# Performance work log

Hardware: AMD Instinct MI355X
Metric: run time of the kernel (lower is better)

Reference implementation:

```python
import jax, jax.numpy as jnp
import numpy as np

TEMPERATURE = 0.5

def setup_inputs() -> dict:
    key = jax.random.key(0)
    k1, k2, k3 = jax.random.split(key, 3)
    B, C, T = 32, 64, 4096
    M, D = 512, 64
    x = jax.random.normal(k1, (B, C, T), dtype=jnp.float32)
    u = jax.random.uniform(k2, (B, T, M), dtype=jnp.float32)
    # nn.init.uniform_(weight, -1/M, 1/M)
    weight = jax.random.uniform(k3, (M, D), dtype=jnp.float32,
                                minval=-1.0 / M, maxval=1.0 / M)
    return {"x": x, "u": u, "weight": weight}

def reference(x, u, weight):
    B, C, T = x.shape
    M, D = weight.shape
    xt = jnp.transpose(x, (0, 2, 1))            # (B, T, D)
    x_flat = xt.reshape(-1, D)                  # (B*T, D)
    distances = (jnp.sum(weight ** 2, axis=1)[None, :]
                 + jnp.sum(x_flat ** 2, axis=1, keepdims=True)
                 - 2.0 * (x_flat @ weight.T)).reshape(B, T, M)
    logits = -distances
    # RelaxedOneHotCategorical(0.5, logits).rsample()
    uu = jnp.clip(u, 1e-9, 1.0 - 1e-9)
    gumbel = -jnp.log(-jnp.log(uu))
    samples = jax.nn.softmax((logits + gumbel) / TEMPERATURE, axis=-1)  # (B,T,M)
    quantized = samples @ weight                # (B, T, D)
    # KL to uniform prior: probs * (log_probs + log M), zero where probs == 0
    log_probs = jax.nn.log_softmax(logits, axis=-1)
    probs = jnp.exp(log_probs)
    KL = jnp.where(probs == 0, 0.0, probs * (log_probs + jnp.log(jnp.float32(M))))
    KL = jnp.mean(jnp.sum(KL, axis=(1, 2)))
    avg_probs = jnp.mean(samples, axis=(0, 1))  # (M,)
    perplexity = jnp.exp(-jnp.sum(avg_probs * jnp.log(avg_probs + 1e-10)))
    return quantized, KL, perplexity
```

## Files before the change

kernel.cpp:

```cpp
#include <hip/hip_runtime.h>
#include <hip/hip_bf16.h>
#include <math.h>


#define LOG_M   6.2383246250395075f
#define EXPM36  2.3195228e-16f

typedef __attribute__((ext_vector_type(8))) __bf16 bf16x8;
typedef __attribute__((ext_vector_type(4))) float  floatx4;

__device__ __forceinline__ unsigned int f2bf_bits(float f) {
    unsigned int b = __builtin_bit_cast(unsigned int, f);
    return (b + 0x7fffu + ((b >> 16) & 1u)) >> 16;
}
__device__ __forceinline__ float bf2f(unsigned int bits16) {
    return __builtin_bit_cast(float, bits16 << 16);
}

__global__ void vq_prep(const float* __restrict__ W,
                        unsigned short* __restrict__ Wbf,
                        unsigned short* __restrict__ WTbf,
                        float* __restrict__ wn2)
{
    const int m = blockIdx.x * 256 + threadIdx.x;
    float acc = 0.f;
    #pragma unroll 8
    for (int d = 0; d < 64; ++d) {
        float v = W[m * 64 + d];
        acc = fmaf(v, v, acc);
        unsigned short h = (unsigned short)f2bf_bits(v);
        Wbf[m * 64 + d]  = h;
        WTbf[d * 512 + m] = h;
    }
    wn2[m] = acc;
}

__global__ __launch_bounds__(256, 3) void vq_main(
    const float* __restrict__ x, const float* __restrict__ u,
    const unsigned short* __restrict__ Wbf, const unsigned short* __restrict__ WTbf,
    const float* __restrict__ wn2, float* __restrict__ out,
    float* __restrict__ avg_g, float* __restrict__ kl_g)
{
    __shared__ __align__(16) unsigned short xs[64][72];
    __shared__ __align__(16) unsigned short sbuf[4][16][40];
    __shared__ float avg_lds[512];

    const int tid  = threadIdx.x;
    const int bid  = blockIdx.x;
    const int b    = bid >> 6;
    const int t0   = (bid & 63) << 6;
    const int w    = tid >> 6;
    const int lane = tid & 63;
    const int ln   = lane & 15;
    const int q    = lane >> 4;

    avg_lds[tid]       = 0.0f;
    avg_lds[tid + 256] = 0.0f;

    #pragma unroll
    for (int k2 = 0; k2 < 16; ++k2) {
        int idx = k2 * 256 + tid;
        int d = idx >> 6, t = idx & 63;
        float v = x[((size_t)(b * 64 + d)) * 4096 + (size_t)(t0 + t)];
        xs[t][d] = (unsigned short)f2bf_bits(v);
    }
    __syncthreads();

    const int tg = t0 + 16 * w + ln;

    bf16x8 xb0 = *(const bf16x8*)&xs[16 * w + ln][q * 8];
    bf16x8 xb1 = *(const bf16x8*)&xs[16 * w + ln][32 + q * 8];

    unsigned int spk[64];
    float T1 = 0.f, T2 = 0.f, Zg = 0.f;
    const float* ub = u + ((size_t)(b * 4096 + tg)) * 512 + 4 * q;

    #pragma unroll
    for (int i = 0; i < 32; ++i) {
        const unsigned short* wrow = Wbf + (size_t)(16 * i + ln) * 64 + q * 8;
        bf16x8 a0 = *(const bf16x8*)(wrow);
        bf16x8 a1 = *(const bf16x8*)(wrow + 32);
        float4 uv = *(const float4*)(ub + 16 * i);
        const float4 wv = *(const float4*)(wn2 + 16 * i + 4 * q);

        floatx4 acc = 0.0f;
        acc = __builtin_amdgcn_mfma_f32_16x16x32_bf16(a0, xb0, acc, 0, 0, 0);
        acc = __builtin_amdgcn_mfma_f32_16x16x32_bf16(a1, xb1, acc, 0, 0, 0);

        float sr[4];
        const float ua[4] = {uv.x, uv.y, uv.z, uv.w};
        const float wa[4] = {wv.x, wv.y, wv.z, wv.w};
        #pragma unroll
        for (int r = 0; r < 4; ++r) {
            float l = fmaf(2.0f, acc[r], -wa[r]);
            float e = __expf(l);
            T1 += e;
            T2 = fmaf(l, e, T2);
            float uu = fmaxf(ua[r], 1e-9f);
            float z = uu - 1.0f;
            float p = fmaf(z, -0.125f, 0.14285715f);
            p = fmaf(z, p, -0.16666667f);
            p = fmaf(z, p, 0.2f);
            p = fmaf(z, p, -0.25f);
            p = fmaf(z, p, 0.33333334f);
            p = fmaf(z, p, -0.5f);
            p = fmaf(z, p, 1.0f);
            float il = (uu > 0.75f) ? (z * p) : __logf(uu);
            float rr = e * __builtin_amdgcn_rcpf(il);
            float s = (rr * rr) * EXPM36;
            Zg += s;
            sr[r] = s;
        }
        spk[2 * i]     = f2bf_bits(sr[0]) | (f2bf_bits(sr[1]) << 16);
        spk[2 * i + 1] = f2bf_bits(sr[2]) | (f2bf_bits(sr[3]) << 16);
    }

    T1 += __shfl_xor(T1, 16); T1 += __shfl_xor(T1, 32);
    T2 += __shfl_xor(T2, 16); T2 += __shfl_xor(T2, 32);
    Zg += __shfl_xor(Zg, 16); Zg += __shfl_xor(Zg, 32);

    float klw = T2 / T1 - logf(T1) + LOG_M;
    klw += __shfl_xor(klw, 1);  klw += __shfl_xor(klw, 2);
    klw += __shfl_xor(klw, 4);  klw += __shfl_xor(klw, 8);
    klw += __shfl_xor(klw, 16); klw += __shfl_xor(klw, 32);
    if (lane == 0) atomicAdd(kl_g, 0.25f * klw);

    const float invZ = 1.0f / Zg;

    floatx4 C2[4];
    #pragma unroll
    for (int dt = 0; dt < 4; ++dt) C2[dt] = 0.0f;

    #pragma unroll
    for (int kk = 0; kk < 16; ++kk) {
        #pragma unroll
        for (int ii = 0; ii < 2; ++ii) {
            const int i = 2 * kk + ii;
            uint2 pk;
            pk.x = spk[2 * i];
            pk.y = spk[2 * i + 1];
            *(uint2*)&sbuf[w][ln][16 * ii + 4 * q] = pk;
            float v0 = bf2f(pk.x & 0xffffu) * invZ;
            float v1 = bf2f(pk.x >> 16)     * invZ;
            float v2 = bf2f(pk.y & 0xffffu) * invZ;
            float v3 = bf2f(pk.y >> 16)     * invZ;
            v0 += __shfl_xor(v0,1); v0 += __shfl_xor(v0,2); v0 += __shfl_xor(v0,4); v0 += __shfl_xor(v0,8);
            v1 += __shfl_xor(v1,1); v1 += __shfl_xor(v1,2); v1 += __shfl_xor(v1,4); v1 += __shfl_xor(v1,8);
            v2 += __shfl_xor(v2,1); v2 += __shfl_xor(v2,2); v2 += __shfl_xor(v2,4); v2 += __shfl_xor(v2,8);
            v3 += __shfl_xor(v3,1); v3 += __shfl_xor(v3,2); v3 += __shfl_xor(v3,4); v3 += __shfl_xor(v3,8);
            if (ln == 0) {
                atomicAdd(&avg_lds[16*i + 4*q + 0], v0);
                atomicAdd(&avg_lds[16*i + 4*q + 1], v1);
                atomicAdd(&avg_lds[16*i + 4*q + 2], v2);
                atomicAdd(&avg_lds[16*i + 4*q + 3], v3);
            }
        }
        __asm__ volatile("s_waitcnt lgkmcnt(0)" ::: "memory");
        bf16x8 sb = *(const bf16x8*)&sbuf[w][ln][8 * q];
        #pragma unroll
        for (int dt = 0; dt < 4; ++dt) {
            bf16x8 a = *(const bf16x8*)(WTbf + (size_t)(16 * dt + ln) * 512 + 32 * kk + 8 * q);
            C2[dt] = __builtin_amdgcn_mfma_f32_16x16x32_bf16(a, sb, C2[dt], 0, 0, 0);
        }
    }

    float* op = out + ((size_t)(b * 4096 + tg)) * 64 + 4 * q;
    #pragma unroll
    for (int dt = 0; dt < 4; ++dt) {
        floatx4 c = C2[dt];
        c[0] *= invZ; c[1] *= invZ; c[2] *= invZ; c[3] *= invZ;
        *(floatx4*)(op + 16 * dt) = c;
    }

    __syncthreads();
    atomicAdd(&avg_g[tid],       avg_lds[tid]);
    atomicAdd(&avg_g[tid + 256], avg_lds[tid + 256]);
}

__global__ void vq_fin(const float* __restrict__ avg_g, const float* __restrict__ kl_g,
                       float* __restrict__ out)
{
    const int lane = threadIdx.x;
    float acc = 0.f;
    #pragma unroll
    for (int k = 0; k < 8; ++k) {
        float a = avg_g[lane * 8 + k] * (1.0f / 131072.0f);
        acc += a * logf(a + 1e-10f);
    }
    acc += __shfl_xor(acc, 1);  acc += __shfl_xor(acc, 2);
    acc += __shfl_xor(acc, 4);  acc += __shfl_xor(acc, 8);
    acc += __shfl_xor(acc, 16); acc += __shfl_xor(acc, 32);
    if (lane == 0) {
        out[8388608] = kl_g[0] * (1.0f / 32.0f);
        out[8388609] = expf(-acc);
    }
}

extern "C" void kernel_launch(void* const* d_in, const int* in_sizes, int n_in,
                              void* d_out, int out_size, void* d_ws, size_t ws_size,
                              hipStream_t stream)
{
    const float* x = (const float*)d_in[0];
    const float* u = (const float*)d_in[1];
    const float* W = (const float*)d_in[2];
    float* out = (float*)d_out;

    char* ws = (char*)d_ws;
    unsigned short* Wbf  = (unsigned short*)(ws);
    unsigned short* WTbf = (unsigned short*)(ws + 65536);
    float* wn2   = (float*)(ws + 131072);
    float* avg_g = (float*)(ws + 133120);
    float* kl_g  = (float*)(ws + 135168);

    (void)hipMemsetAsync(ws + 133120, 0, 2048 + 64, stream);

    vq_prep<<<dim3(2),    dim3(256), 0, stream>>>(W, Wbf, WTbf, wn2);
    vq_main<<<dim3(2048), dim3(256), 0, stream>>>(x, u, Wbf, WTbf, wn2, out, avg_g, kl_g);
    vq_fin <<<dim3(1),    dim3(64),  0, stream>>>(avg_g, kl_g, out);
}
```

Measured before the change: 570.1 us.

## Split fused VQ kernel into sampling and quantize passes via global buffer

The single fused kernel is split in two. The first kernel computes the Gumbel-softmax samples and writes them as bf16 to a large workspace buffer, along with per-row inverse normalizers. The second kernel reads them back to run the quantize matmul and the codebook-average reduction. This removes the 64-register packed sample array and the 3-waves launch bound, aiming for higher occupancy. The cost is about 256MB of extra global write and read traffic. It also swaps shuffle reductions for DPP row sums, shards the global atomics across 16 slots, and replaces the memset with zeroing inside the prep kernel. The new path only runs when the workspace is large enough; otherwise the old fused path is kept.

```diff
diff --git a/kernel.cpp b/kernel.cpp
--- a/kernel.cpp
+++ b/kernel.cpp
@@ -16,11 +16,27 @@
 __device__ __forceinline__ float bf2f(unsigned int bits16) {
     return __builtin_bit_cast(float, bits16 << 16);
 }
+template <int CTRL>
+__device__ __forceinline__ float dpp_add(float v) {
+    int t = __builtin_amdgcn_update_dpp(0, __builtin_bit_cast(int, v),
+                                        CTRL, 0xF, 0xF, true);
+    return v + __builtin_bit_cast(float, t);
+}
+__device__ __forceinline__ float row16_sum(float v) {
+    v = dpp_add<0xB1>(v);
+    v = dpp_add<0x4E>(v);
+    v = dpp_add<0x124>(v);
+    v = dpp_add<0x128>(v);
+    return v;
+}
 
 __global__ void vq_prep(const float* __restrict__ W,
                         unsigned short* __restrict__ Wbf,
                         unsigned short* __restrict__ WTbf,
-                        float* __restrict__ wn2)
+                        float* __restrict__ wn2,
+                        float* __restrict__ avg_sh,
+                        float* __restrict__ kl_sh,
+                        int zero_mode)
 {
     const int m = blockIdx.x * 256 + threadIdx.x;
     float acc = 0.f;
@@ -33,6 +49,206 @@
         WTbf[d * 512 + m] = h;
     }
     wn2[m] = acc;
+    if (zero_mode) {
+        #pragma unroll
+        for (int j = 0; j < 16; ++j) avg_sh[m * 16 + j] = 0.f;
+        kl_sh[m * 2]     = 0.f;
+        kl_sh[m * 2 + 1] = 0.f;
+    }
+}
+
+__global__ __launch_bounds__(256, 4) void vq_samp(
+    const float* __restrict__ x, const float* __restrict__ u,
+    const unsigned short* __restrict__ Wbf,
+    const float* __restrict__ wn2,
+    unsigned short* __restrict__ Sblk,
+    float* __restrict__ invZg,
+    float* __restrict__ kl_sh)
+{
+    __shared__ __align__(16) unsigned short xs[64][72];
+    __shared__ __align__(16) unsigned short sbuf[4][16][40];
+
+    const int tid  = threadIdx.x;
+    const int bid  = blockIdx.x;
+    const int b    = bid >> 6;
+    const int t0   = (bid & 63) << 6;
+    const int w    = tid >> 6;
+    const int lane = tid & 63;
+    const int ln   = lane & 15;
+    const int q    = lane >> 4;
+
+    #pragma unroll
+    for (int k2 = 0; k2 < 16; ++k2) {
+        int idx = k2 * 256 + tid;
+        int d = idx >> 6, t = idx & 63;
+        float v = x[((size_t)(b * 64 + d)) * 4096 + (size_t)(t0 + t)];
+        xs[t][d] = (unsigned short)f2bf_bits(v);
+    }
+    __syncthreads();
+
+    const int tg = t0 + 16 * w + ln;
+
+    bf16x8 xb0 = *(const bf16x8*)&xs[16 * w + ln][q * 8];
+    bf16x8 xb1 = *(const bf16x8*)&xs[16 * w + ln][32 + q * 8];
+
+    float T1 = 0.f, T2 = 0.f, Zg = 0.f;
+    const float* ub = u + ((size_t)(b * 4096 + tg)) * 512 + 4 * q;
+
+    #pragma unroll 2
+    for (int kk = 0; kk < 16; ++kk) {
+        #pragma unroll
+        for (int ii = 0; ii < 2; ++ii) {
+            const int i = 2 * kk + ii;
+            const unsigned short* wrow = Wbf + (size_t)(16 * i + ln) * 64 + q * 8;
+            bf16x8 a0 = *(const bf16x8*)(wrow);
+            bf16x8 a1 = *(const bf16x8*)(wrow + 32);
+            float4 uv = *(const float4*)(ub + 16 * i);
+            const float4 wv = *(const float4*)(wn2 + 16 * i + 4 * q);
+
+            floatx4 acc = 0.0f;
+            acc = __builtin_amdgcn_mfma_f32_16x16x32_bf16(a0, xb0, acc, 0, 0, 0);
+            acc = __builtin_amdgcn_mfma_f32_16x16x32_bf16(a1, xb1, acc, 0, 0, 0);
+
+            float sr[4];
+            const float ua[4] = {uv.x, uv.y, uv.z, uv.w};
+            const float wa[4] = {wv.x, wv.y, wv.z, wv.w};
+            #pragma unroll
+            for (int r = 0; r < 4; ++r) {
+                float l = fmaf(2.0f, acc[r], -wa[r]);
+                float e = __expf(l);
+                T1 += e;
+                T2 = fmaf(l, e, T2);
+                float uu = fmaxf(ua[r], 1e-9f);
+                float z = uu - 1.0f;
+                float p = fmaf(z, -0.125f, 0.14285715f);
+                p = fmaf(z, p, -0.16666667f);
+                p = fmaf(z, p, 0.2f);
+                p = fmaf(z, p, -0.25f);
+                p = fmaf(z, p, 0.33333334f);
+                p = fmaf(z, p, -0.5f);
+                p = fmaf(z, p, 1.0f);
+                float il = (uu > 0.75f) ? (z * p) : __logf(uu);
+                float rr = e * __builtin_amdgcn_rcpf(il);
+                float s = (rr * rr) * EXPM36;
+                Zg += s;
+                sr[r] = s;
+            }
+            *(uint2*)&sbuf[w][ln][16 * ii + 4 * q] = make_uint2(
+                f2bf_bits(sr[0]) | (f2bf_bits(sr[1]) << 16),
+                f2bf_bits(sr[2]) | (f2bf_bits(sr[3]) << 16));
+        }
+        __asm__ volatile("s_waitcnt lgkmcnt(0)" ::: "memory");
+        uint4 sv = *(const uint4*)&sbuf[w][ln][8 * q];
+        *(uint4*)(Sblk + (((size_t)bid * 16 + kk) * 4 + w) * 512 + lane * 8) = sv;
+    }
+
+    T1 += __shfl_xor(T1, 16); T1 += __shfl_xor(T1, 32);
+    T2 += __shfl_xor(T2, 16); T2 += __shfl_xor(T2, 32);
+    Zg += __shfl_xor(Zg, 16); Zg += __shfl_xor(Zg, 32);
+
+    float klw = T2 / T1 - logf(T1) + LOG_M;
+    klw += __shfl_xor(klw, 1);  klw += __shfl_xor(klw, 2);
+    klw += __shfl_xor(klw, 4);  klw += __shfl_xor(klw, 8);
+    klw += __shfl_xor(klw, 16); klw += __shfl_xor(klw, 32);
+    if (lane == 0)
+        atomicAdd(&kl_sh[((bid * 4 + w) & 15) * 64], 0.25f * klw);
+
+    if (q == 0) invZg[(size_t)b * 4096 + tg] = 1.0f / Zg;
+}
+
+__global__ __launch_bounds__(256, 4) void vq_qnt(
+    const unsigned short* __restrict__ Sblk,
+    const unsigned short* __restrict__ WTbf,
+    const float* __restrict__ invZg,
+    float* __restrict__ out,
+    float* __restrict__ avg_sh)
+{
+    __shared__ float avg_wv[4][512];
+
+    const int tid  = threadIdx.x;
+    const int bid  = blockIdx.x;
+    const int b    = bid >> 6;
+    const int t0   = (bid & 63) << 6;
+    const int w    = tid >> 6;
+    const int lane = tid & 63;
+    const int ln   = lane & 15;
+    const int q    = lane >> 4;
+    const int tg   = t0 + 16 * w + ln;
+
+    const float invZ = invZg[(size_t)b * 4096 + tg];
+
+    floatx4 C2[4];
+    #pragma unroll
+    for (int dt = 0; dt < 4; ++dt) C2[dt] = 0.0f;
+
+    #pragma unroll 4
+    for (int kk = 0; kk < 16; ++kk) {
+        uint4 sv = *(const uint4*)(Sblk + (((size_t)bid * 16 + kk) * 4 + w) * 512 + lane * 8);
+        bf16x8 sb = __builtin_bit_cast(bf16x8, sv);
+
+        float p0 = bf2f(sv.x & 0xffffu) * invZ;
+        float p1 = bf2f(sv.x >> 16)     * invZ;
+        float p2 = bf2f(sv.y & 0xffffu) * invZ;
+        float p3 = bf2f(sv.y >> 16)     * invZ;
+        float p4 = bf2f(sv.z & 0xffffu) * invZ;
+        float p5 = bf2f(sv.z >> 16)     * invZ;
+        float p6 = bf2f(sv.w & 0xffffu) * invZ;
+        float p7 = bf2f(sv.w >> 16)     * invZ;
+        p0 = row16_sum(p0); p1 = row16_sum(p1); p2 = row16_sum(p2); p3 = row16_sum(p3);
+        p4 = row16_sum(p4); p5 = row16_sum(p5); p6 = row16_sum(p6); p7 = row16_sum(p7);
+        if (ln == 0) {
+            *(float4*)&avg_wv[w][32 * kk + 8 * q]     = make_float4(p0, p1, p2, p3);
+            *(float4*)&avg_wv[w][32 * kk + 8 * q + 4] = make_float4(p4, p5, p6, p7);
+        }
+
+        #pragma unroll
+        for (int dt = 0; dt < 4; ++dt) {
+            bf16x8 a = *(const bf16x8*)(WTbf + (size_t)(16 * dt + ln) * 512 + 32 * kk + 8 * q);
+            C2[dt] = __builtin_amdgcn_mfma_f32_16x16x32_bf16(a, sb, C2[dt], 0, 0, 0);
+        }
+    }
+
+    float* op = out + ((size_t)(b * 4096 + tg)) * 64 + 4 * q;
+    #pragma unroll
+    for (int dt = 0; dt < 4; ++dt) {
+        floatx4 c = C2[dt];
+        c[0] *= invZ; c[1] *= invZ; c[2] *= invZ; c[3] *= invZ;
+        *(floatx4*)(op + 16 * dt) = c;
+    }
+
+    __syncthreads();
+    #pragma unroll
+    for (int mm = tid; mm < 512; mm += 256) {
+        float s = avg_wv[0][mm] + avg_wv[1][mm] + avg_wv[2][mm] + avg_wv[3][mm];
+        atomicAdd(&avg_sh[(bid & 15) * 512 + mm], s);
+    }
+}
+
+__global__ void vq_fin1(const float* __restrict__ avg_sh,
+                        const float* __restrict__ kl_sh,
+                        float* __restrict__ out)
+{
+    const int lane = threadIdx.x;
+    float acc = 0.f;
+    #pragma unroll
+    for (int k = 0; k < 8; ++k) {
+        float a = 0.f;
+        #pragma unroll
+        for (int c = 0; c < 16; ++c) a += avg_sh[c * 512 + lane * 8 + k];
+        a *= (1.0f / 131072.0f);
+        acc += a * logf(a + 1e-10f);
+    }
+    float kv = (lane < 16) ? kl_sh[lane * 64] : 0.f;
+    acc += __shfl_xor(acc, 1);  acc += __shfl_xor(acc, 2);
+    acc += __shfl_xor(acc, 4);  acc += __shfl_xor(acc, 8);
+    acc += __shfl_xor(acc, 16); acc += __shfl_xor(acc, 32);
+    kv  += __shfl_xor(kv, 1);   kv  += __shfl_xor(kv, 2);
+    kv  += __shfl_xor(kv, 4);   kv  += __shfl_xor(kv, 8);
+    kv  += __shfl_xor(kv, 16);  kv  += __shfl_xor(kv, 32);
+    if (lane == 0) {
+        out[8388608] = kv * (1.0f / 32.0f);
+        out[8388609] = expf(-acc);
+    }
 }
 
 __global__ __launch_bounds__(256, 3) void vq_main(
@@ -177,8 +393,8 @@
     atomicAdd(&avg_g[tid + 256], avg_lds[tid + 256]);
 }
 
-__global__ void vq_fin(const float* __restrict__ avg_g, const float* __restrict__ kl_g,
-                       float* __restrict__ out)
+__global__ void vq_fin0(const float* __restrict__ avg_g, const float* __restrict__ kl_g,
+                        float* __restrict__ out)
 {
     const int lane = threadIdx.x;
     float acc = 0.f;
@@ -209,12 +425,30 @@
     unsigned short* Wbf  = (unsigned short*)(ws);
     unsigned short* WTbf = (unsigned short*)(ws + 65536);
     float* wn2   = (float*)(ws + 131072);
-    float* avg_g = (float*)(ws + 133120);
-    float* kl_g  = (float*)(ws + 135168);
-
-    (void)hipMemsetAsync(ws + 133120, 0, 2048 + 64, stream);
-
-    vq_prep<<<dim3(2),    dim3(256), 0, stream>>>(W, Wbf, WTbf, wn2);
-    vq_main<<<dim3(2048), dim3(256), 0, stream>>>(x, u, Wbf, WTbf, wn2, out, avg_g, kl_g);
-    vq_fin <<<dim3(1),    dim3(64),  0, stream>>>(avg_g, kl_g, out);
-}
+
+    const size_t NEED = 1048576ull + 134217728ull;
+
+    if (ws_size >= NEED) {
+        float* avg_sh = (float*)(ws + 133120);
+        float* kl_sh  = (float*)(ws + 165888);
+        float* invZg  = (float*)(ws + 169984);
+        unsigned short* Sblk = (unsigned short*)(ws + 1048576);
+
+        vq_prep<<<dim3(2),    dim3(256), 0, stream>>>(W, Wbf, WTbf, wn2,
+                                                      avg_sh, kl_sh, 1);
+        vq_samp<<<dim3(2048), dim3(256), 0, stream>>>(x, u, Wbf, wn2,
+                                                      Sblk, invZg, kl_sh);
+        vq_qnt <<<dim3(2048), dim3(256), 0, stream>>>(Sblk, WTbf, invZg,
+                                                      out, avg_sh);
+        vq_fin1<<<dim3(1),    dim3(64),  0, stream>>>(avg_sh, kl_sh, out);
+    } else {
+        float* avg_g = (float*)(ws + 133120);
+        float* kl_g  = (float*)(ws + 135168);
+        (void)hipMemsetAsync(ws + 133120, 0, 2048 + 64, stream);
+        vq_prep<<<dim3(2),    dim3(256), 0, stream>>>(W, Wbf, WTbf, wn2,
+                                                      avg_g, kl_g, 0);
+        vq_main<<<dim3(2048), dim3(256), 0, stream>>>(x, u, Wbf, WTbf, wn2,
+                                                      out, avg_g, kl_g);
+        vq_fin0<<<dim3(1),    dim3(64),  0, stream>>>(avg_g, kl_g, out);
+    }
+}
```

After: 504.1 us. 11.6% less time.

## Split codebook across waves per 16-token block and shard global atomics

Applied to the files above, without the earlier changes.

Each block now handles 16 tokens, and its four waves each cover a 128-entry slice of the codebook. This replaces the old layout of 64 tokens per block with each wave sweeping all 512 entries. Softmax statistics and the second-GEMM partial outputs are combined through LDS. The per-column average reduction uses DPP row sums and plain LDS stores instead of shuffles plus LDS atomics. Global atomics are spread over 32 avg shards and 64 KL slots, which the prep kernel zeroes in place of the memset. The change cuts register pressure (occupancy 3→4) and raises the grid to 8192 blocks, at the cost of extra syncthreads and an LDS round-trip for the partial outputs.

```diff
diff --git a/kernel.cpp b/kernel.cpp
--- a/kernel.cpp
+++ b/kernel.cpp
@@ -16,11 +16,26 @@
 __device__ __forceinline__ float bf2f(unsigned int bits16) {
     return __builtin_bit_cast(float, bits16 << 16);
 }
+template <int CTRL>
+__device__ __forceinline__ float dpp_add(float v) {
+    int t = __builtin_amdgcn_update_dpp(0, __builtin_bit_cast(int, v),
+                                        CTRL, 0xF, 0xF, true);
+    return v + __builtin_bit_cast(float, t);
+}
+__device__ __forceinline__ float row16_sum(float v) {
+    v = dpp_add<0xB1>(v);
+    v = dpp_add<0x4E>(v);
+    v = dpp_add<0x124>(v);
+    v = dpp_add<0x128>(v);
+    return v;
+}
 
 __global__ void vq_prep(const float* __restrict__ W,
                         unsigned short* __restrict__ Wbf,
                         unsigned short* __restrict__ WTbf,
-                        float* __restrict__ wn2)
+                        float* __restrict__ wn2,
+                        float* __restrict__ avg_sh,
+                        float* __restrict__ kl_sh)
 {
     const int m = blockIdx.x * 256 + threadIdx.x;
     float acc = 0.f;
@@ -33,55 +48,58 @@
         WTbf[d * 512 + m] = h;
     }
     wn2[m] = acc;
-}
-
-__global__ __launch_bounds__(256, 3) void vq_main(
+    #pragma unroll
+    for (int j = 0; j < 32; ++j) avg_sh[j * 512 + m] = 0.f;
+    if (m < 64) kl_sh[m] = 0.f;
+}
+
+__global__ __launch_bounds__(256, 4) void vq_fused(
     const float* __restrict__ x, const float* __restrict__ u,
     const unsigned short* __restrict__ Wbf, const unsigned short* __restrict__ WTbf,
     const float* __restrict__ wn2, float* __restrict__ out,
-    float* __restrict__ avg_g, float* __restrict__ kl_g)
-{
-    __shared__ __align__(16) unsigned short xs[64][72];
+    float* __restrict__ avg_sh, float* __restrict__ kl_sh)
+{
+    __shared__ __align__(16) unsigned short xs[16][72];
     __shared__ __align__(16) unsigned short sbuf[4][16][40];
+    __shared__ float red[4][3][16];
+    __shared__ __align__(16) float c2r[4][64][20];
     __shared__ float avg_lds[512];
 
     const int tid  = threadIdx.x;
     const int bid  = blockIdx.x;
-    const int b    = bid >> 6;
-    const int t0   = (bid & 63) << 6;
+    const int b    = bid >> 8;
+    const int t0   = (bid & 255) << 4;
     const int w    = tid >> 6;
     const int lane = tid & 63;
     const int ln   = lane & 15;
     const int q    = lane >> 4;
-
-    avg_lds[tid]       = 0.0f;
-    avg_lds[tid + 256] = 0.0f;
-
-    #pragma unroll
-    for (int k2 = 0; k2 < 16; ++k2) {
+    const int m0   = 128 * w;
+
+    #pragma unroll
+    for (int k2 = 0; k2 < 4; ++k2) {
         int idx = k2 * 256 + tid;
-        int d = idx >> 6, t = idx & 63;
+        int d = idx >> 4, t = idx & 15;
         float v = x[((size_t)(b * 64 + d)) * 4096 + (size_t)(t0 + t)];
         xs[t][d] = (unsigned short)f2bf_bits(v);
     }
     __syncthreads();
 
-    const int tg = t0 + 16 * w + ln;
-
-    bf16x8 xb0 = *(const bf16x8*)&xs[16 * w + ln][q * 8];
-    bf16x8 xb1 = *(const bf16x8*)&xs[16 * w + ln][32 + q * 8];
-
-    unsigned int spk[64];
+    const int tg = t0 + ln;
+
+    bf16x8 xb0 = *(const bf16x8*)&xs[ln][q * 8];
+    bf16x8 xb1 = *(const bf16x8*)&xs[ln][32 + q * 8];
+
+    unsigned int spk[16];
     float T1 = 0.f, T2 = 0.f, Zg = 0.f;
-    const float* ub = u + ((size_t)(b * 4096 + tg)) * 512 + 4 * q;
-
-    #pragma unroll
-    for (int i = 0; i < 32; ++i) {
-        const unsigned short* wrow = Wbf + (size_t)(16 * i + ln) * 64 + q * 8;
+    const float* ub = u + ((size_t)(b * 4096 + tg)) * 512 + m0 + 4 * q;
+
+    #pragma unroll
+    for (int i = 0; i < 8; ++i) {
+        const unsigned short* wrow = Wbf + (size_t)(m0 + 16 * i + ln) * 64 + q * 8;
         bf16x8 a0 = *(const bf16x8*)(wrow);
         bf16x8 a1 = *(const bf16x8*)(wrow + 32);
         float4 uv = *(const float4*)(ub + 16 * i);
-        const float4 wv = *(const float4*)(wn2 + 16 * i + 4 * q);
+        const float4 wv = *(const float4*)(wn2 + m0 + 16 * i + 4 * q);
 
         floatx4 acc = 0.0f;
         acc = __builtin_amdgcn_mfma_f32_16x16x32_bf16(a0, xb0, acc, 0, 0, 0);
@@ -118,80 +136,108 @@
     T1 += __shfl_xor(T1, 16); T1 += __shfl_xor(T1, 32);
     T2 += __shfl_xor(T2, 16); T2 += __shfl_xor(T2, 32);
     Zg += __shfl_xor(Zg, 16); Zg += __shfl_xor(Zg, 32);
-
-    float klw = T2 / T1 - logf(T1) + LOG_M;
-    klw += __shfl_xor(klw, 1);  klw += __shfl_xor(klw, 2);
-    klw += __shfl_xor(klw, 4);  klw += __shfl_xor(klw, 8);
-    klw += __shfl_xor(klw, 16); klw += __shfl_xor(klw, 32);
-    if (lane == 0) atomicAdd(kl_g, 0.25f * klw);
-
-    const float invZ = 1.0f / Zg;
+    if (q == 0) {
+        red[w][0][ln] = T1;
+        red[w][1][ln] = T2;
+        red[w][2][ln] = Zg;
+    }
+    __syncthreads();
+
+    const float T1t = red[0][0][ln] + red[1][0][ln] + red[2][0][ln] + red[3][0][ln];
+    const float T2t = red[0][1][ln] + red[1][1][ln] + red[2][1][ln] + red[3][1][ln];
+    const float Zgt = red[0][2][ln] + red[1][2][ln] + red[2][2][ln] + red[3][2][ln];
+    const float invZ = 1.0f / Zgt;
+
+    if (w == 0) {
+        float klw = T2t / T1t - logf(T1t) + LOG_M;
+        klw += __shfl_xor(klw, 1);  klw += __shfl_xor(klw, 2);
+        klw += __shfl_xor(klw, 4);  klw += __shfl_xor(klw, 8);
+        klw += __shfl_xor(klw, 16); klw += __shfl_xor(klw, 32);
+        if (lane == 0) atomicAdd(&kl_sh[bid & 63], 0.25f * klw);
+    }
 
     floatx4 C2[4];
     #pragma unroll
     for (int dt = 0; dt < 4; ++dt) C2[dt] = 0.0f;
 
     #pragma unroll
-    for (int kk = 0; kk < 16; ++kk) {
+    for (int kk = 0; kk < 4; ++kk) {
         #pragma unroll
         for (int ii = 0; ii < 2; ++ii) {
             const int i = 2 * kk + ii;
-            uint2 pk;
-            pk.x = spk[2 * i];
-            pk.y = spk[2 * i + 1];
-            *(uint2*)&sbuf[w][ln][16 * ii + 4 * q] = pk;
-            float v0 = bf2f(pk.x & 0xffffu) * invZ;
-            float v1 = bf2f(pk.x >> 16)     * invZ;
-            float v2 = bf2f(pk.y & 0xffffu) * invZ;
-            float v3 = bf2f(pk.y >> 16)     * invZ;
-            v0 += __shfl_xor(v0,1); v0 += __shfl_xor(v0,2); v0 += __shfl_xor(v0,4); v0 += __shfl_xor(v0,8);
-            v1 += __shfl_xor(v1,1); v1 += __shfl_xor(v1,2); v1 += __shfl_xor(v1,4); v1 += __shfl_xor(v1,8);
-            v2 += __shfl_xor(v2,1); v2 += __shfl_xor(v2,2); v2 += __shfl_xor(v2,4); v2 += __shfl_xor(v2,8);
-            v3 += __shfl_xor(v3,1); v3 += __shfl_xor(v3,2); v3 += __shfl_xor(v3,4); v3 += __shfl_xor(v3,8);
-            if (ln == 0) {
-                atomicAdd(&avg_lds[16*i + 4*q + 0], v0);
-                atomicAdd(&avg_lds[16*i + 4*q + 1], v1);
-                atomicAdd(&avg_lds[16*i + 4*q + 2], v2);
-                atomicAdd(&avg_lds[16*i + 4*q + 3], v3);
-            }
+            *(uint2*)&sbuf[w][ln][16 * ii + 4 * q] =
+                make_uint2(spk[2 * i], spk[2 * i + 1]);
         }
         __asm__ volatile("s_waitcnt lgkmcnt(0)" ::: "memory");
-        bf16x8 sb = *(const bf16x8*)&sbuf[w][ln][8 * q];
+        uint4 sv = *(const uint4*)&sbuf[w][ln][8 * q];
+        bf16x8 sb = __builtin_bit_cast(bf16x8, sv);
+
+        float p0 = bf2f(sv.x & 0xffffu) * invZ;
+        float p1 = bf2f(sv.x >> 16)     * invZ;
+        float p2 = bf2f(sv.y & 0xffffu) * invZ;
+        float p3 = bf2f(sv.y >> 16)     * invZ;
+        float p4 = bf2f(sv.z & 0xffffu) * invZ;
+        float p5 = bf2f(sv.z >> 16)     * invZ;
+        float p6 = bf2f(sv.w & 0xffffu) * invZ;
+        float p7 = bf2f(sv.w >> 16)     * invZ;
+        p0 = row16_sum(p0); p1 = row16_sum(p1); p2 = row16_sum(p2); p3 = row16_sum(p3);
+        p4 = row16_sum(p4); p5 = row16_sum(p5); p6 = row16_sum(p6); p7 = row16_sum(p7);
+        if (ln == 0) {
+            *(float4*)&avg_lds[m0 + 32 * kk + 8 * q]     = make_float4(p0, p1, p2, p3);
+            *(float4*)&avg_lds[m0 + 32 * kk + 8 * q + 4] = make_float4(p4, p5, p6, p7);
+        }
+
         #pragma unroll
         for (int dt = 0; dt < 4; ++dt) {
-            bf16x8 a = *(const bf16x8*)(WTbf + (size_t)(16 * dt + ln) * 512 + 32 * kk + 8 * q);
+            bf16x8 a = *(const bf16x8*)(WTbf + (size_t)(16 * dt + ln) * 512
+                                        + m0 + 32 * kk + 8 * q);
             C2[dt] = __builtin_amdgcn_mfma_f32_16x16x32_bf16(a, sb, C2[dt], 0, 0, 0);
         }
     }
 
-    float* op = out + ((size_t)(b * 4096 + tg)) * 64 + 4 * q;
-    #pragma unroll
-    for (int dt = 0; dt < 4; ++dt) {
-        floatx4 c = C2[dt];
-        c[0] *= invZ; c[1] *= invZ; c[2] *= invZ; c[3] *= invZ;
-        *(floatx4*)(op + 16 * dt) = c;
-    }
-
+    #pragma unroll
+    for (int dt = 0; dt < 4; ++dt)
+        *(floatx4*)&c2r[w][lane][4 * dt] = C2[dt];
     __syncthreads();
-    atomicAdd(&avg_g[tid],       avg_lds[tid]);
-    atomicAdd(&avg_g[tid + 256], avg_lds[tid + 256]);
-}
-
-__global__ void vq_fin(const float* __restrict__ avg_g, const float* __restrict__ kl_g,
+
+    floatx4 cf = *(const floatx4*)&c2r[0][lane][4 * w];
+    {
+        floatx4 c1 = *(const floatx4*)&c2r[1][lane][4 * w];
+        floatx4 c2 = *(const floatx4*)&c2r[2][lane][4 * w];
+        floatx4 c3 = *(const floatx4*)&c2r[3][lane][4 * w];
+        #pragma unroll
+        for (int r = 0; r < 4; ++r)
+            cf[r] = (cf[r] + c1[r] + c2[r] + c3[r]) * invZ;
+    }
+    *(floatx4*)(out + ((size_t)(b * 4096 + tg)) * 64 + 16 * w + 4 * q) = cf;
+
+    atomicAdd(&avg_sh[(bid & 31) * 512 + tid],       avg_lds[tid]);
+    atomicAdd(&avg_sh[(bid & 31) * 512 + tid + 256], avg_lds[tid + 256]);
+}
+
+__global__ void vq_fin(const float* __restrict__ avg_sh,
+                       const float* __restrict__ kl_sh,
                        float* __restrict__ out)
 {
     const int lane = threadIdx.x;
     float acc = 0.f;
     #pragma unroll
     for (int k = 0; k < 8; ++k) {
-        float a = avg_g[lane * 8 + k] * (1.0f / 131072.0f);
+        float a = 0.f;
+        #pragma unroll
+        for (int c = 0; c < 32; ++c) a += avg_sh[c * 512 + lane * 8 + k];
+        a *= (1.0f / 131072.0f);
         acc += a * logf(a + 1e-10f);
     }
+    float kv = kl_sh[lane];
     acc += __shfl_xor(acc, 1);  acc += __shfl_xor(acc, 2);
     acc += __shfl_xor(acc, 4);  acc += __shfl_xor(acc, 8);
     acc += __shfl_xor(acc, 16); acc += __shfl_xor(acc, 32);
+    kv  += __shfl_xor(kv, 1);   kv  += __shfl_xor(kv, 2);
+    kv  += __shfl_xor(kv, 4);   kv  += __shfl_xor(kv, 8);
+    kv  += __shfl_xor(kv, 16);  kv  += __shfl_xor(kv, 32);
     if (lane == 0) {
-        out[8388608] = kl_g[0] * (1.0f / 32.0f);
+        out[8388608] = kv * (1.0f / 32.0f);
         out[8388609] = expf(-acc);
     }
 }
@@ -208,13 +254,12 @@
     char* ws = (char*)d_ws;
     unsigned short* Wbf  = (unsigned short*)(ws);
     unsigned short* WTbf = (unsigned short*)(ws + 65536);
-    float* wn2   = (float*)(ws + 131072);
-    float* avg_g = (float*)(ws + 133120);
-    float* kl_g  = (float*)(ws + 135168);
-
-    (void)hipMemsetAsync(ws + 133120, 0, 2048 + 64, stream);
-
-    vq_prep<<<dim3(2),    dim3(256), 0, stream>>>(W, Wbf, WTbf, wn2);
-    vq_main<<<dim3(2048), dim3(256), 0, stream>>>(x, u, Wbf, WTbf, wn2, out, avg_g, kl_g);
-    vq_fin <<<dim3(1),    dim3(64),  0, stream>>>(avg_g, kl_g, out);
-}
+    float* wn2    = (float*)(ws + 131072);
+    float* avg_sh = (float*)(ws + 133120);
+    float* kl_sh  = (float*)(ws + 198656);
+
+    vq_prep <<<dim3(2),    dim3(256), 0, stream>>>(W, Wbf, WTbf, wn2, avg_sh, kl_sh);
+    vq_fused<<<dim3(8192), dim3(256), 0, stream>>>(x, u, Wbf, WTbf, wn2,
+                                                   out, avg_sh, kl_sh);
+    vq_fin  <<<dim3(1),    dim3(64),  0, stream>>>(avg_sh, kl_sh, out);
+}
```

Result: faster. 500.8 us (-12.2%).
